# Optimization experiments

Hardware: AMD Instinct MI355X
Metric: run time of the kernel (lower is better)

## Reference

```python
import jax, jax.numpy as jnp
import numpy as np

N_NODES = 50000
N_EDGES = 800000
NFEAT, NHID, NOUT = 512, 256, 64


def setup_inputs() -> dict:
    key = jax.random.key(0)
    ks = jax.random.split(key, 8)
    x = jax.random.normal(ks[0], (N_NODES, NFEAT), dtype=jnp.float32)
    w1 = jax.random.normal(ks[1], (NFEAT, NHID), dtype=jnp.float32) * (1.0 / np.sqrt(NFEAT))
    b1 = jnp.zeros((NHID,), dtype=jnp.float32)
    w2 = jax.random.normal(ks[2], (NHID, NOUT), dtype=jnp.float32) * (1.0 / np.sqrt(NHID))
    b2 = jnp.zeros((NOUT,), dtype=jnp.float32)
    edge_w = jax.random.uniform(ks[3], (N_EDGES,), dtype=jnp.float32)
    row = jnp.sort(jax.random.randint(ks[4], (N_EDGES,), 0, N_NODES, dtype=jnp.int32))
    col = jax.random.randint(ks[5], (N_EDGES,), 0, N_NODES, dtype=jnp.int32)
    return {"x": x, "w1": w1, "b1": b1, "w2": w2, "b2": b2,
            "edge_w": edge_w, "row": row, "col": col}


def _spmm(edge_w, row, col, h, n_nodes):
    # sparse adj (COO) @ dense h : gather source rows, scale, scatter-add to dest
    msgs = h[col] * edge_w[:, None]          # [E, d]
    return jax.ops.segment_sum(msgs, row, num_segments=n_nodes)


def reference(x, w1, b1, w2, b2, edge_w, row, col):
    n = x.shape[0]
    # layer 1: support = x @ W1; out = adj @ support + b1; relu
    h = jnp.matmul(x, w1)                    # [N, nhid]
    h = _spmm(edge_w, row, col, h, n) + b1
    h = jax.nn.relu(h)
    # layer 2
    h = jnp.matmul(h, w2)                    # [N, nout]
    out = _spmm(edge_w, row, col, h, n) + b2
    return out
```

## Files before the change

### kernel.cpp

```cpp
#include <hip/hip_runtime.h>

#define N_NODES 50000
#define MP      50048
#define N_EDGES 800000
#define NFEAT   512
#define NHID    256
#define NOUT    64

typedef __bf16 bf16x8 __attribute__((ext_vector_type(8)));
typedef float  f32x4  __attribute__((ext_vector_type(4)));

#define GLOAD_LDS16(g, l) __builtin_amdgcn_global_load_lds(                    \
    (const __attribute__((address_space(1))) void*)(g),                        \
    (__attribute__((address_space(3))) void*)(l), 16, 0, 0)

__device__ __forceinline__ unsigned short f2bf(float f) {
    __bf16 b = (__bf16)f;
    return __builtin_bit_cast(unsigned short, b);
}

__global__ __launch_bounds__(256) void prep(const int* __restrict__ row,
                                            int* __restrict__ rp,
                                            const float* __restrict__ w1,
                                            __bf16* __restrict__ w1t,
                                            const float* __restrict__ w2,
                                            __bf16* __restrict__ w2t,
                                            __bf16* __restrict__ h1) {
    const int b = blockIdx.x, t = threadIdx.x;
    if (b < 196) {
        int r = b * 256 + t;
        if (r <= N_NODES) {
            int lo = 0, hi = N_EDGES;
            while (lo < hi) {
                int mid = (lo + hi) >> 1;
                if (row[mid] < r) lo = mid + 1; else hi = mid;
            }
            rp[r] = lo;
        }
    } else if (b < 708) {
        int o = (b - 196) * 256 + t;
        w1t[o] = (__bf16)w1[(size_t)(o & 511) * NHID + (o >> 9)];
    } else if (b < 772) {
        int o = (b - 708) * 256 + t;
        w2t[o] = (__bf16)w2[(size_t)(o & 255) * NOUT + (o >> 8)];
    } else {
        int o = (b - 772) * 256 + t;
        h1[(size_t)N_NODES * NHID + o] = (__bf16)0.f;
    }
}

__global__ __launch_bounds__(256) void gemm1_fused(const float* __restrict__ X,
                                                   const __bf16* __restrict__ Bt,
                                                   __bf16* __restrict__ C) {
    __shared__ __bf16 As[128 * 32];
    __shared__ __bf16 Bs[256 * 32];
    const int t = threadIdx.x;
    const int w = t >> 6, l = t & 63;
    const int wm = w >> 1, wn = w & 1;
    const int ml = l & 15, quad = l >> 4;
    const int row0 = blockIdx.x * 128;

    f32x4 acc[4][8] = {};

    for (int k0 = 0; k0 < NFEAT; k0 += 32) {
        #pragma unroll
        for (int it = 0; it < 4; it++) {
            int q = it * 256 + w * 64 + l;
            int r = q >> 2, cc = (q & 3) * 8;
            GLOAD_LDS16(Bt + (size_t)r * NFEAT + k0 + cc,
                        Bs + (size_t)(it * 256 + w * 64) * 8);
        }
        #pragma unroll
        for (int it = 0; it < 2; it++) {
            int q = it * 256 + t;
            int r = q >> 2, cc = (q & 3) * 8;
            int gr = row0 + r;
            unsigned short u[8];
            if (gr < N_NODES) {
                const float* src = X + (size_t)gr * NFEAT + k0 + cc;
                float4 a = *(const float4*)src;
                float4 b = *(const float4*)(src + 4);
                u[0] = f2bf(a.x); u[1] = f2bf(a.y); u[2] = f2bf(a.z); u[3] = f2bf(a.w);
                u[4] = f2bf(b.x); u[5] = f2bf(b.y); u[6] = f2bf(b.z); u[7] = f2bf(b.w);
            } else {
                #pragma unroll
                for (int j = 0; j < 8; j++) u[j] = 0;
            }
            uint4 o;
            o.x = (unsigned)u[0] | ((unsigned)u[1] << 16);
            o.y = (unsigned)u[2] | ((unsigned)u[3] << 16);
            o.z = (unsigned)u[4] | ((unsigned)u[5] << 16);
            o.w = (unsigned)u[6] | ((unsigned)u[7] << 16);
            *(uint4*)(As + (size_t)q * 8) = o;
        }
        __syncthreads();

        bf16x8 af[4], bfr[8];
        #pragma unroll
        for (int mi = 0; mi < 4; mi++)
            af[mi] = *(const bf16x8*)(As + (wm * 64 + mi * 16 + ml) * 32 + quad * 8);
        #pragma unroll
        for (int ni = 0; ni < 8; ni++)
            bfr[ni] = *(const bf16x8*)(Bs + (wn * 128 + ni * 16 + ml) * 32 + quad * 8);
        #pragma unroll
        for (int mi = 0; mi < 4; mi++)
            #pragma unroll
            for (int ni = 0; ni < 8; ni++)
                acc[mi][ni] = __builtin_amdgcn_mfma_f32_16x16x32_bf16(
                    af[mi], bfr[ni], acc[mi][ni], 0, 0, 0);
        __syncthreads();
    }

    #pragma unroll
    for (int mi = 0; mi < 4; mi++) {
        int gr = row0 + wm * 64 + mi * 16 + quad * 4;
        #pragma unroll
        for (int ni = 0; ni < 8; ni++) {
            int gc = wn * 128 + ni * 16 + ml;
            #pragma unroll
            for (int r2 = 0; r2 < 4; r2++)
                C[(size_t)(gr + r2) * NHID + gc] = (__bf16)acc[mi][ni][r2];
        }
    }
}

__global__ __launch_bounds__(256) void gemm2_mfma(const __bf16* __restrict__ A,
                                                  const __bf16* __restrict__ Bt,
                                                  __bf16* __restrict__ C) {
    __shared__ __bf16 As[128 * 32];
    __shared__ __bf16 Bs[64 * 32];
    const int t = threadIdx.x;
    const int w = t >> 6, l = t & 63;
    const int ml = l & 15, quad = l >> 4;
    const int row0 = blockIdx.x * 128;

    f32x4 acc[2][4] = {};

    for (int k0 = 0; k0 < NHID; k0 += 32) {
        #pragma unroll
        for (int i = 0; i < 2; i++) {
            int q = (w * 2 + i) * 64 + l;
            int r = q >> 2, cc = (q & 3) * 8;
            GLOAD_LDS16(A + (size_t)(row0 + r) * NHID + k0 + cc, As + (w * 2 + i) * 512);
        }
        {
            int q = w * 64 + l;
            int r = q >> 2, cc = (q & 3) * 8;
            GLOAD_LDS16(Bt + (size_t)r * NHID + k0 + cc, Bs + w * 512);
        }
        __syncthreads();
        bf16x8 af[2], bfr[4];
        #pragma unroll
        for (int mi = 0; mi < 2; mi++)
            af[mi] = *(const bf16x8*)(As + (w * 32 + mi * 16 + ml) * 32 + quad * 8);
        #pragma unroll
        for (int ni = 0; ni < 4; ni++)
            bfr[ni] = *(const bf16x8*)(Bs + (ni * 16 + ml) * 32 + quad * 8);
        #pragma unroll
        for (int mi = 0; mi < 2; mi++)
            #pragma unroll
            for (int ni = 0; ni < 4; ni++)
                acc[mi][ni] = __builtin_amdgcn_mfma_f32_16x16x32_bf16(
                    af[mi], bfr[ni], acc[mi][ni], 0, 0, 0);
        __syncthreads();
    }

    #pragma unroll
    for (int mi = 0; mi < 2; mi++) {
        int gr = row0 + w * 32 + mi * 16 + quad * 4;
        #pragma unroll
        for (int ni = 0; ni < 4; ni++) {
            int gc = ni * 16 + ml;
            #pragma unroll
            for (int r2 = 0; r2 < 4; r2++)
                C[(size_t)(gr + r2) * NOUT + gc] = (__bf16)acc[mi][ni][r2];
        }
    }
}

__global__ __launch_bounds__(256) void spmm1_wave(const __bf16* __restrict__ h0,
                                                  const float* __restrict__ ew,
                                                  const int* __restrict__ col,
                                                  const int* __restrict__ rp,
                                                  const float* __restrict__ b1,
                                                  __bf16* __restrict__ h1) {
    const int n    = blockIdx.x * 4 + (threadIdx.x >> 6);
    const int lane = threadIdx.x & 63;
    const int half = lane >> 5;
    const int fl   = lane & 31;
    const int s = rp[n], e = rp[n + 1];

    float acc[8] = {};
    int i = s + half;
    for (; i + 6 < e; i += 8) {
        int   c0 = col[i],     c1 = col[i + 2], c2 = col[i + 4], c3 = col[i + 6];
        float w0 = ew[i],      w1 = ew[i + 2],  w2 = ew[i + 4],  w3 = ew[i + 6];
        uint4 v0 = *(const uint4*)(h0 + (size_t)c0 * NHID + fl * 8);
        uint4 v1 = *(const uint4*)(h0 + (size_t)c1 * NHID + fl * 8);
        uint4 v2 = *(const uint4*)(h0 + (size_t)c2 * NHID + fl * 8);
        uint4 v3 = *(const uint4*)(h0 + (size_t)c3 * NHID + fl * 8);
        const unsigned* p0 = &v0.x; const unsigned* p1 = &v1.x;
        const unsigned* p2 = &v2.x; const unsigned* p3 = &v3.x;
        #pragma unroll
        for (int j = 0; j < 4; j++) {
            acc[2*j+0] += w0 * __builtin_bit_cast(float, p0[j] << 16)
                        + w1 * __builtin_bit_cast(float, p1[j] << 16)
                        + w2 * __builtin_bit_cast(float, p2[j] << 16)
                        + w3 * __builtin_bit_cast(float, p3[j] << 16);
            acc[2*j+1] += w0 * __builtin_bit_cast(float, p0[j] & 0xffff0000u)
                        + w1 * __builtin_bit_cast(float, p1[j] & 0xffff0000u)
                        + w2 * __builtin_bit_cast(float, p2[j] & 0xffff0000u)
                        + w3 * __builtin_bit_cast(float, p3[j] & 0xffff0000u);
        }
    }
    for (; i < e; i += 2) {
        int   c0 = col[i];
        float w0 = ew[i];
        uint4 v0 = *(const uint4*)(h0 + (size_t)c0 * NHID + fl * 8);
        const unsigned* p0 = &v0.x;
        #pragma unroll
        for (int j = 0; j < 4; j++) {
            acc[2*j+0] += w0 * __builtin_bit_cast(float, p0[j] << 16);
            acc[2*j+1] += w0 * __builtin_bit_cast(float, p0[j] & 0xffff0000u);
        }
    }

    #pragma unroll
    for (int j = 0; j < 8; j++)
        acc[j] += __shfl_down(acc[j], 32, 64);

    if (half == 0) {
        unsigned short u[8];
        #pragma unroll
        for (int j = 0; j < 8; j++) {
            float v = acc[j] + b1[fl * 8 + j];
            u[j] = f2bf(v > 0.f ? v : 0.f);
        }
        uint4 o;
        o.x = (unsigned)u[0] | ((unsigned)u[1] << 16);
        o.y = (unsigned)u[2] | ((unsigned)u[3] << 16);
        o.z = (unsigned)u[4] | ((unsigned)u[5] << 16);
        o.w = (unsigned)u[6] | ((unsigned)u[7] << 16);
        *(uint4*)(h1 + (size_t)n * NHID + fl * 8) = o;
    }
}

__global__ __launch_bounds__(256) void spmm2_wave(const __bf16* __restrict__ h2,
                                                  const float* __restrict__ ew,
                                                  const int* __restrict__ col,
                                                  const int* __restrict__ rp,
                                                  const float* __restrict__ b2,
                                                  float* __restrict__ out) {
    const int n    = blockIdx.x * 4 + (threadIdx.x >> 6);
    const int lane = threadIdx.x & 63;
    const int g    = lane >> 4;
    const int fl   = lane & 15;
    const int s = rp[n], e = rp[n + 1];

    float a0 = 0.f, a1 = 0.f, a2 = 0.f, a3 = 0.f;
    int i = s + g;
    for (; i + 4 < e; i += 8) {
        int   c0 = col[i];     float w0 = ew[i];
        int   c1 = col[i + 4]; float w1 = ew[i + 4];
        uint2 v0 = *(const uint2*)(h2 + (size_t)c0 * NOUT + fl * 4);
        uint2 v1 = *(const uint2*)(h2 + (size_t)c1 * NOUT + fl * 4);
        a0 += w0 * __builtin_bit_cast(float, v0.x << 16)
            + w1 * __builtin_bit_cast(float, v1.x << 16);
        a1 += w0 * __builtin_bit_cast(float, v0.x & 0xffff0000u)
            + w1 * __builtin_bit_cast(float, v1.x & 0xffff0000u);
        a2 += w0 * __builtin_bit_cast(float, v0.y << 16)
            + w1 * __builtin_bit_cast(float, v1.y << 16);
        a3 += w0 * __builtin_bit_cast(float, v0.y & 0xffff0000u)
            + w1 * __builtin_bit_cast(float, v1.y & 0xffff0000u);
    }
    for (; i < e; i += 4) {
        int   c0 = col[i]; float w0 = ew[i];
        uint2 v0 = *(const uint2*)(h2 + (size_t)c0 * NOUT + fl * 4);
        a0 += w0 * __builtin_bit_cast(float, v0.x << 16);
        a1 += w0 * __builtin_bit_cast(float, v0.x & 0xffff0000u);
        a2 += w0 * __builtin_bit_cast(float, v0.y << 16);
        a3 += w0 * __builtin_bit_cast(float, v0.y & 0xffff0000u);
    }

    a0 += __shfl_down(a0, 32, 64); a1 += __shfl_down(a1, 32, 64);
    a2 += __shfl_down(a2, 32, 64); a3 += __shfl_down(a3, 32, 64);
    a0 += __shfl_down(a0, 16, 64); a1 += __shfl_down(a1, 16, 64);
    a2 += __shfl_down(a2, 16, 64); a3 += __shfl_down(a3, 16, 64);

    if (lane < 16) {
        float4 bb = *(const float4*)(b2 + fl * 4);
        float4 o = make_float4(a0 + bb.x, a1 + bb.y, a2 + bb.z, a3 + bb.w);
        *(float4*)(out + (size_t)n * NOUT + fl * 4) = o;
    }
}

extern "C" void kernel_launch(void* const* d_in, const int* in_sizes, int n_in,
                              void* d_out, int out_size, void* d_ws, size_t ws_size,
                              hipStream_t stream) {
    const float* x   = (const float*)d_in[0];
    const float* w1  = (const float*)d_in[1];
    const float* b1  = (const float*)d_in[2];
    const float* w2  = (const float*)d_in[3];
    const float* b2  = (const float*)d_in[4];
    const float* ew  = (const float*)d_in[5];
    const int*   row = (const int*)d_in[6];
    const int*   col = (const int*)d_in[7];
    float* out = (float*)d_out;

    char* ws = (char*)d_ws;
    size_t off = 0;
    int*    rp  = (int*)(ws + off);   off += 256 * 1024;
    __bf16* w1t = (__bf16*)(ws + off); off += (size_t)NHID * NFEAT * 2;
    __bf16* w2t = (__bf16*)(ws + off); off += (size_t)NOUT * NHID * 2;
    __bf16* h0  = (__bf16*)(ws + off); off += (size_t)MP * NHID * 2;
    __bf16* h1  = (__bf16*)(ws + off); off += (size_t)MP * NHID * 2;
    __bf16* h2  = (__bf16*)(ws + off);

    prep<<<820, 256, 0, stream>>>(row, rp, w1, w1t, w2, w2t, h1);

    gemm1_fused<<<MP / 128, 256, 0, stream>>>(x, w1t, h0);

    spmm1_wave<<<N_NODES / 4, 256, 0, stream>>>(h0, ew, col, rp, b1, h1);

    gemm2_mfma<<<MP / 128, 256, 0, stream>>>(h1, w2t, h2);

    spmm2_wave<<<N_NODES / 4, 256, 0, stream>>>(h2, ew, col, rp, b2, out);
}
```

Before: 298.3 us.

## Halve gemm1 M-tile and prefetch next X slice into registers

Measured after the change: 281.4 us. -5.6%, faster.

```diff
diff --git a/kernel.cpp b/kernel.cpp
--- a/kernel.cpp
+++ b/kernel.cpp
@@ -52,15 +52,24 @@
 __global__ __launch_bounds__(256) void gemm1_fused(const float* __restrict__ X,
                                                    const __bf16* __restrict__ Bt,
                                                    __bf16* __restrict__ C) {
-    __shared__ __bf16 As[128 * 32];
+    __shared__ __bf16 As[64 * 32];
     __shared__ __bf16 Bs[256 * 32];
     const int t = threadIdx.x;
     const int w = t >> 6, l = t & 63;
     const int wm = w >> 1, wn = w & 1;
     const int ml = l & 15, quad = l >> 4;
-    const int row0 = blockIdx.x * 128;
-
-    f32x4 acc[4][8] = {};
+    const int row0 = blockIdx.x * 64;
+
+    const int ar = t >> 2;
+    const int ac = (t & 3) * 8;
+    const int agr = row0 + ar;
+    const bool aval = (agr < N_NODES);
+    const float* asrc = X + (size_t)agr * NFEAT + ac;
+
+    f32x4 acc[2][8] = {};
+
+    float4 pa = make_float4(0.f, 0.f, 0.f, 0.f), pb = pa;
+    if (aval) { pa = *(const float4*)asrc; pb = *(const float4*)(asrc + 4); }
 
     for (int k0 = 0; k0 < NFEAT; k0 += 32) {
         #pragma unroll
@@ -70,40 +79,30 @@
             GLOAD_LDS16(Bt + (size_t)r * NFEAT + k0 + cc,
                         Bs + (size_t)(it * 256 + w * 64) * 8);
         }
-        #pragma unroll
-        for (int it = 0; it < 2; it++) {
-            int q = it * 256 + t;
-            int r = q >> 2, cc = (q & 3) * 8;
-            int gr = row0 + r;
-            unsigned short u[8];
-            if (gr < N_NODES) {
-                const float* src = X + (size_t)gr * NFEAT + k0 + cc;
-                float4 a = *(const float4*)src;
-                float4 b = *(const float4*)(src + 4);
-                u[0] = f2bf(a.x); u[1] = f2bf(a.y); u[2] = f2bf(a.z); u[3] = f2bf(a.w);
-                u[4] = f2bf(b.x); u[5] = f2bf(b.y); u[6] = f2bf(b.z); u[7] = f2bf(b.w);
-            } else {
-                #pragma unroll
-                for (int j = 0; j < 8; j++) u[j] = 0;
-            }
+        {
             uint4 o;
-            o.x = (unsigned)u[0] | ((unsigned)u[1] << 16);
-            o.y = (unsigned)u[2] | ((unsigned)u[3] << 16);
-            o.z = (unsigned)u[4] | ((unsigned)u[5] << 16);
-            o.w = (unsigned)u[6] | ((unsigned)u[7] << 16);
-            *(uint4*)(As + (size_t)q * 8) = o;
+            o.x = (unsigned)f2bf(pa.x) | ((unsigned)f2bf(pa.y) << 16);
+            o.y = (unsigned)f2bf(pa.z) | ((unsigned)f2bf(pa.w) << 16);
+            o.z = (unsigned)f2bf(pb.x) | ((unsigned)f2bf(pb.y) << 16);
+            o.w = (unsigned)f2bf(pb.z) | ((unsigned)f2bf(pb.w) << 16);
+            *(uint4*)(As + (size_t)t * 8) = o;
         }
         __syncthreads();
 
-        bf16x8 af[4], bfr[8];
-        #pragma unroll
-        for (int mi = 0; mi < 4; mi++)
-            af[mi] = *(const bf16x8*)(As + (wm * 64 + mi * 16 + ml) * 32 + quad * 8);
+        if (k0 + 32 < NFEAT && aval) {
+            pa = *(const float4*)(asrc + k0 + 32);
+            pb = *(const float4*)(asrc + k0 + 36);
+        }
+
+        bf16x8 af[2], bfr[8];
+        #pragma unroll
+        for (int mi = 0; mi < 2; mi++)
+            af[mi] = *(const bf16x8*)(As + (wm * 32 + mi * 16 + ml) * 32 + quad * 8);
         #pragma unroll
         for (int ni = 0; ni < 8; ni++)
             bfr[ni] = *(const bf16x8*)(Bs + (wn * 128 + ni * 16 + ml) * 32 + quad * 8);
         #pragma unroll
-        for (int mi = 0; mi < 4; mi++)
+        for (int mi = 0; mi < 2; mi++)
             #pragma unroll
             for (int ni = 0; ni < 8; ni++)
                 acc[mi][ni] = __builtin_amdgcn_mfma_f32_16x16x32_bf16(
@@ -112,8 +111,8 @@
     }
 
     #pragma unroll
-    for (int mi = 0; mi < 4; mi++) {
-        int gr = row0 + wm * 64 + mi * 16 + quad * 4;
+    for (int mi = 0; mi < 2; mi++) {
+        int gr = row0 + wm * 32 + mi * 16 + quad * 4;
         #pragma unroll
         for (int ni = 0; ni < 8; ni++) {
             int gc = wn * 128 + ni * 16 + ml;
@@ -318,7 +317,7 @@
 
     prep<<<820, 256, 0, stream>>>(row, rp, w1, w1t, w2, w2t, h1);
 
-    gemm1_fused<<<MP / 128, 256, 0, stream>>>(x, w1t, h0);
+    gemm1_fused<<<MP / 64, 256, 0, stream>>>(x, w1t, h0);
 
     spmm1_wave<<<N_NODES / 4, 256, 0, stream>>>(h0, ew, col, rp, b1, h1);
 
```
